# Kernel optimization log

Measured on AMD Instinct MI355X. Metric: run time of the kernel, lower is better.

## Reference

```python
import jax, jax.numpy as jnp
import numpy as np

B, L, C = 4, 8192, 256
HEADS = 1
DP = C // HEADS
FFN_HID = C * 2 * 4  # (d_model*2) * ffn_dim_expansion
EPS = 1e-5


def _layernorm(x, gamma, beta):
    mu = jnp.mean(x, axis=-1, keepdims=True)
    var = jnp.var(x, axis=-1, keepdims=True)
    return (x - mu) * jax.lax.rsqrt(var + EPS) * gamma + beta


def setup_inputs() -> dict:
    key = jax.random.key(0)
    ks = jax.random.split(key, 12)
    s = 0.02
    return {
        "source": jax.random.normal(ks[0], (B, L, C), jnp.float32),
        "target": jax.random.normal(ks[1], (B, L, C), jnp.float32),
        "Wq": jax.random.normal(ks[2], (C, C), jnp.float32) * s,
        "Wk": jax.random.normal(ks[3], (C, C), jnp.float32) * s,
        "Wv": jax.random.normal(ks[4], (C, C), jnp.float32) * s,
        "Wl": jax.random.normal(ks[5], (C, C), jnp.float32) * s,
        "gamma1": jnp.ones((C,), jnp.float32),
        "beta1": jnp.zeros((C,), jnp.float32),
        "W1": jax.random.normal(ks[6], (2 * C, FFN_HID), jnp.float32) * s,
        "b1": jnp.zeros((FFN_HID,), jnp.float32),
        "W2": jax.random.normal(ks[7], (FFN_HID, C), jnp.float32) * s,
        "b2": jnp.zeros((C,), jnp.float32),
        "gamma2": jnp.ones((C,), jnp.float32),
        "beta2": jnp.zeros((C,), jnp.float32),
        "h": 64,
        "w": 128,
    }


def reference(source, target, Wq, Wk, Wv, Wl, gamma1, beta1, W1, b1, W2, b2,
              gamma2, beta2, h, w):
    assert L == h * w
    q = (source @ Wq).reshape(B, L, HEADS, DP)
    k = (target @ Wk).reshape(B, L, HEADS, DP)
    v = (target @ Wv).reshape(B, L, HEADS, DP)
    k = jax.nn.softmax(k, axis=1)  # softmax over token dim
    context = jnp.einsum('bnhd,bnhe->bhde', q, k)   # small d×d per head
    attn = jnp.einsum('bhde,bnhe->bnhd', context, v).reshape(B, L, C)
    message = _layernorm(attn @ Wl, gamma1, beta1)
    hidden = jax.nn.gelu(jnp.concatenate([source, message], axis=-1) @ W1 + b1,
                         approximate=False)
    message = _layernorm(hidden @ W2 + b2, gamma2, beta2)
    return source + message
```

## Files before the change

### kernel.cpp

```cpp
#include <hip/hip_runtime.h>
#include <hip/hip_bf16.h>

typedef unsigned short u16;
typedef __attribute__((ext_vector_type(8))) short short8;
typedef __attribute__((ext_vector_type(4))) float f32x4;

#define B_    4
#define L_    8192
#define C_    256
#define BL_   (B_*L_)
#define BLC_  (BL_*C_)
#define FFN_  2048
#define EPS_  1e-5f

#define GLDS(dst, src) __builtin_amdgcn_global_load_lds( \
    (const __attribute__((address_space(1))) unsigned int*)(src), \
    (__attribute__((address_space(3))) unsigned int*)(dst), 16, 0, 0)

__device__ __forceinline__ float bf2f(u16 v) {
  union { unsigned int u; float f; } x; x.u = ((unsigned int)v) << 16; return x.f;
}
__device__ __forceinline__ u16 f2bf(float f) {
  union { float f; unsigned int u; } x; x.f = f;
  unsigned int lsb = (x.u >> 16) & 1u;
  return (u16)((x.u + 0x7fffu + lsb) >> 16);
}
__device__ __forceinline__ float gelu_f(float x) {
  float z = fabsf(x) * 0.70710678118654752f;
  float t = __builtin_amdgcn_rcpf(1.f + 0.3275911f * z);
  float p = ((((1.061405429f * t - 1.453152027f) * t + 1.421413741f) * t
              - 0.284496736f) * t + 0.254829592f) * t;
  float e = __expf(-z * z);
  float erfv = copysignf(1.f - p * e, x);
  return 0.5f * x * (1.f + erfv);
}

template<int MODE, int ACT, int SPLITK>
__launch_bounds__(256, 2)
__global__ void gemm_abt(const u16* __restrict__ A0, const u16* __restrict__ A1,
                         int SEL, int lda,
                         const u16* __restrict__ Bt,
                         const float* __restrict__ bias,
                         u16* __restrict__ Cb, float* __restrict__ Cf,
                         int M, int N, int K,
                         long sAb, long sBb, long sCb)
{
  __shared__ __align__(16) u16 As[2 * 128 * 32];
  __shared__ __align__(16) u16 Bs[2 * 128 * 32];

  const int mtiles = M >> 7;
  const int tile = blockIdx.x;
  const int mt0 = (tile % mtiles) << 7;
  const int nt0 = (tile / mtiles) << 7;
  const int kchunk = K / (int)gridDim.y;
  const int k0beg = blockIdx.y * kchunk;
  const int k0end = k0beg + kchunk;
  const int bz = blockIdx.z;
  A0 += (long)bz * sAb;  A1 += (long)bz * sAb;  Bt += (long)bz * sBb;

  const u16* Abase = (MODE == 2 && nt0 >= SEL) ? A1 : A0;

  const int tid  = threadIdx.x;
  const int wave = tid >> 6, lane = tid & 63;
  const int srow = lane >> 2;
  const int gq   = (lane & 3) ^ (srow & 3);
  const int frow = lane & 15;
  const int fq   = lane >> 4;
  const int fqx  = (fq ^ (frow & 3)) * 8;

  f32x4 zero = {0.f, 0.f, 0.f, 0.f};
  f32x4 acc[4][4];
#pragma unroll
  for (int i = 0; i < 4; i++)
#pragma unroll
    for (int j = 0; j < 4; j++) acc[i][j] = zero;

  const int wm = (wave & 1) * 64, wn = (wave >> 1) * 64;

  for (int k0 = k0beg; k0 < k0end; k0 += 64) {
    __syncthreads();
    const u16* Asrc;
    int ka;
    if (MODE == 1) {
      const bool lo = (k0 < SEL);
      Asrc = lo ? A0 : A1;
      ka = lo ? k0 : (k0 - SEL);
    } else { Asrc = Abase; ka = k0; }
#pragma unroll
    for (int h = 0; h < 2; h++) {
#pragma unroll
      for (int i = 0; i < 2; i++) {
        const int chunk = i * 4 + wave;
        GLDS(&As[h * 4096 + chunk * 512],
             Asrc + (long)(mt0 + chunk * 16 + srow) * lda + (ka + h * 32 + gq * 8));
        GLDS(&Bs[h * 4096 + chunk * 512],
             Bt + (long)(nt0 + chunk * 16 + srow) * K + (k0 + h * 32 + gq * 8));
      }
    }
    __syncthreads();
#pragma unroll
    for (int h = 0; h < 2; h++) {
      short8 af[4], bf[4];
#pragma unroll
      for (int t = 0; t < 4; t++)
        af[t] = *(const short8*)&As[h * 4096 + (wm + t * 16 + frow) * 32 + fqx];
#pragma unroll
      for (int t = 0; t < 4; t++)
        bf[t] = *(const short8*)&Bs[h * 4096 + (wn + t * 16 + frow) * 32 + fqx];
#pragma unroll
      for (int mt = 0; mt < 4; mt++)
#pragma unroll
        for (int nt = 0; nt < 4; nt++)
          acc[mt][nt] = __builtin_amdgcn_mfma_f32_16x16x32_bf16(af[mt], bf[nt], acc[mt][nt], 0, 0, 0);
    }
  }

  if (SPLITK) {
    float* Cp = Cf + (long)bz * sCb;
#pragma unroll
    for (int mt = 0; mt < 4; mt++)
#pragma unroll
      for (int r = 0; r < 4; r++) {
        const int row = mt0 + wm + mt * 16 + fq * 4 + r;
#pragma unroll
        for (int nt = 0; nt < 4; nt++)
          atomicAdd(&Cp[(long)row * N + nt0 + wn + nt * 16 + frow], acc[mt][nt][r]);
      }
  } else {
    u16* Cp = Cb + (long)bz * sCb;
    float bv[4];
#pragma unroll
    for (int nt = 0; nt < 4; nt++)
      bv[nt] = bias ? bias[nt0 + wn + nt * 16 + frow] : 0.f;
#pragma unroll
    for (int mt = 0; mt < 4; mt++)
#pragma unroll
      for (int r = 0; r < 4; r++) {
        const int row = mt0 + wm + mt * 16 + fq * 4 + r;
#pragma unroll
        for (int nt = 0; nt < 4; nt++) {
          float v = acc[mt][nt][r] + bv[nt];
          if (ACT == 1) v = gelu_f(v);
          Cp[(long)row * N + nt0 + wn + nt * 16 + frow] = f2bf(v);
        }
      }
  }
}

template<int CVTB, int OUTF>
__launch_bounds__(256, 3)
__global__ void gemm_ln(const u16* __restrict__ A, long sAb, int lda, int K,
                        const void* __restrict__ Btv, long sBb, int zshift,
                        const float* __restrict__ bias,
                        const float* __restrict__ gamma, const float* __restrict__ beta,
                        const float* __restrict__ src, void* __restrict__ outv,
                        long Moff)
{
  __shared__ __align__(16) u16 As[2 * 64 * 32];
  __shared__ __align__(16) u16 Bs[2 * 256 * 32];
  __shared__ float red_s[64][4], red_q[64][4];

  const int gm0 = blockIdx.x * 64;
  const int z = gm0 >> zshift;
  const int ml = gm0 - (z << zshift);
  A += (long)z * sAb + (long)ml * lda;
  const float* Bf = (const float*)Btv + (CVTB ? (long)z * sBb : 0);
  const u16*   Bb = (const u16*)Btv   + (CVTB ? 0 : (long)z * sBb);

  const int tid = threadIdx.x, wave = tid >> 6, lane = tid & 63;
  const int srow = lane >> 2, gq = (lane & 3) ^ (srow & 3);
  const int frow = lane & 15, fq = lane >> 4;
  const int fqx = (fq ^ (frow & 3)) * 8;
  const int wn = wave * 64;

  f32x4 zero = {0.f, 0.f, 0.f, 0.f};
  f32x4 acc[4][4];
#pragma unroll
  for (int i = 0; i < 4; i++)
#pragma unroll
    for (int j = 0; j < 4; j++) acc[i][j] = zero;

  for (int k0 = 0; k0 < K; k0 += 64) {
    __syncthreads();
#pragma unroll
    for (int h = 0; h < 2; h++) {
      GLDS(&As[h * 2048 + wave * 512],
           A + (long)(wave * 16 + srow) * lda + (k0 + h * 32 + gq * 8));
#pragma unroll
      for (int i = 0; i < 4; i++) {
        const int chunk = i * 4 + wave;
        if (CVTB) {
          const float* bp = Bf + (long)(chunk * 16 + srow) * K + (k0 + h * 32 + gq * 8);
          float4 p0 = *(const float4*)bp;
          float4 p1 = *(const float4*)(bp + 4);
          short8 w;
          w[0] = (short)f2bf(p0.x); w[1] = (short)f2bf(p0.y);
          w[2] = (short)f2bf(p0.z); w[3] = (short)f2bf(p0.w);
          w[4] = (short)f2bf(p1.x); w[5] = (short)f2bf(p1.y);
          w[6] = (short)f2bf(p1.z); w[7] = (short)f2bf(p1.w);
          *(short8*)&Bs[h * 8192 + chunk * 512 + srow * 32 + (lane & 3) * 8] = w;
        } else {
          GLDS(&Bs[h * 8192 + chunk * 512],
               Bb + (long)(chunk * 16 + srow) * K + (k0 + h * 32 + gq * 8));
        }
      }
    }
    __syncthreads();
#pragma unroll
    for (int h = 0; h < 2; h++) {
      short8 af[4], bf[4];
#pragma unroll
      for (int t = 0; t < 4; t++)
        af[t] = *(const short8*)&As[h * 2048 + (t * 16 + frow) * 32 + fqx];
#pragma unroll
      for (int t = 0; t < 4; t++)
        bf[t] = *(const short8*)&Bs[h * 8192 + (wn + t * 16 + frow) * 32 + fqx];
#pragma unroll
      for (int mt = 0; mt < 4; mt++)
#pragma unroll
        for (int nt = 0; nt < 4; nt++)
          acc[mt][nt] = __builtin_amdgcn_mfma_f32_16x16x32_bf16(af[mt], bf[nt], acc[mt][nt], 0, 0, 0);
    }
  }

  float gv[4], bv[4], b2v[4];
#pragma unroll
  for (int nt = 0; nt < 4; nt++) {
    const int col = wn + nt * 16 + frow;
    gv[nt] = gamma[col]; bv[nt] = beta[col];
    b2v[nt] = OUTF ? bias[col] : 0.f;
  }
#pragma unroll
  for (int mt = 0; mt < 4; mt++)
#pragma unroll
    for (int r = 0; r < 4; r++) {
      float s = 0.f, q = 0.f;
#pragma unroll
      for (int nt = 0; nt < 4; nt++) {
        float v = acc[mt][nt][r] + b2v[nt];
        acc[mt][nt][r] = v; s += v; q += v * v;
      }
#pragma unroll
      for (int m = 1; m < 16; m <<= 1) {
        s += __shfl_xor(s, m, 16); q += __shfl_xor(q, m, 16);
      }
      if (frow == 0) {
        const int row = mt * 16 + fq * 4 + r;
        red_s[row][wave] = s; red_q[row][wave] = q;
      }
    }
  __syncthreads();
#pragma unroll
  for (int mt = 0; mt < 4; mt++)
#pragma unroll
    for (int r = 0; r < 4; r++) {
      const int row = mt * 16 + fq * 4 + r;
      float4 ss = *(const float4*)red_s[row];
      float4 qq = *(const float4*)red_q[row];
      const float s = ss.x + ss.y + ss.z + ss.w;
      const float q = qq.x + qq.y + qq.z + qq.w;
      const float mu = s * (1.f / 256.f);
      const float var = q * (1.f / 256.f) - mu * mu;
      const float rs = 1.f / sqrtf(var + EPS_);
      const long grow = Moff + gm0 + row;
#pragma unroll
      for (int nt = 0; nt < 4; nt++) {
        const int col = wn + nt * 16 + frow;
        const float o = (acc[mt][nt][r] - mu) * rs * gv[nt] + bv[nt];
        if (OUTF)
          ((float*)outv)[grow * 256 + col] = o + src[grow * 256 + col];
        else
          ((u16*)outv)[grow * 256 + col] = f2bf(o);
      }
    }
}

__global__ void weightpack(const float* __restrict__ Wq, const float* __restrict__ Wk,
                           const float* __restrict__ Wv, const float* __restrict__ Wl,
                           const float* __restrict__ W1, const float* __restrict__ W2,
                           u16* __restrict__ WqC, u16* __restrict__ WlT,
                           u16* __restrict__ WqkvT, u16* __restrict__ W1T,
                           u16* __restrict__ W2T)
{
  __shared__ u16 t[32][33];
  const int bid = blockIdx.x, tx = threadIdx.x, ty = threadIdx.y;
  const float* in; u16* out; int Cc, R, bx, by;
  if (bid < 256) {
    const int w = bid >> 6, tt = bid & 63;
    bx = (tt & 7) * 32; by = (tt >> 3) * 32; Cc = 256; R = 256;
    if (w == 0) {
#pragma unroll
      for (int i = ty; i < 32; i += 8)
        WqC[(long)(by + i) * 256 + bx + tx] = f2bf(Wq[(long)(by + i) * 256 + bx + tx]);
      return;
    }
    in  = (w == 1) ? Wl : (w == 2) ? Wk : Wv;
    out = (w == 1) ? WlT : (w == 2) ? (WqkvT + 65536) : (WqkvT + 131072);
  } else if (bid < 1280) {
    const int l = bid - 256; bx = (l & 63) * 32; by = (l >> 6) * 32;
    in = W1; out = W1T; Cc = 2048; R = 512;
  } else {
    const int l = bid - 1280; bx = (l & 7) * 32; by = (l >> 3) * 32;
    in = W2; out = W2T; Cc = 256; R = 2048;
  }
#pragma unroll
  for (int i = ty; i < 32; i += 8)
    t[i][tx] = f2bf(in[(long)(by + i) * Cc + bx + tx]);
  __syncthreads();
#pragma unroll
  for (int i = ty; i < 32; i += 8)
    out[(long)(bx + i) * R + by + tx] = t[tx][i];
}

__global__ void castzero(const float* __restrict__ src, const float* __restrict__ tgt,
                         u16* __restrict__ srcB, u16* __restrict__ tgtB,
                         float* __restrict__ Mtf)
{
  const int x = blockIdx.x;
  if (x < BLC_ / 1024) {
    const float* in = blockIdx.y ? tgt : src;
    u16* out = blockIdx.y ? tgtB : srcB;
    const int i = (x * 256 + threadIdx.x) * 4;
    float4 v = *(const float4*)(in + i);
    ushort4 o; o.x = f2bf(v.x); o.y = f2bf(v.y); o.z = f2bf(v.z); o.w = f2bf(v.w);
    *(ushort4*)(out + i) = o;
  } else if (blockIdx.y == 0) {
    const int i = ((x - BLC_ / 1024) * 256 + threadIdx.x) * 4;
    float4 zv = {0.f, 0.f, 0.f, 0.f};
    *(float4*)(Mtf + i) = zv;
  }
}

__global__ void transQK(const u16* __restrict__ QKV,
                        u16* __restrict__ qlT, u16* __restrict__ kT)
{
  __shared__ u16 t[32][33];
  const int z = blockIdx.z, zb = z & 3;
  const u16* in = QKV + (long)zb * L_ * 768 + (z < 4 ? 0 : 256);
  u16* out = (z < 4 ? qlT : kT) + (long)zb * L_ * C_;
  const int bx = blockIdx.x * 32, by = blockIdx.y * 32;
  const int tx = threadIdx.x, ty = threadIdx.y;
#pragma unroll
  for (int i = ty; i < 32; i += 8)
    t[i][tx] = in[(long)(by + i) * 768 + bx + tx];
  __syncthreads();
#pragma unroll
  for (int i = ty; i < 32; i += 8)
    out[(long)(bx + i) * L_ + by + tx] = t[tx][i];
}

__global__ void softmax_rows(u16* __restrict__ data, int rowlen)
{
  const long base = (long)blockIdx.x * rowlen;
  const int tid = threadIdx.x, wave = tid >> 6, lane = tid & 63;
  __shared__ float red[4];

  float m = -3.4e38f;
  for (int i = tid; i < rowlen; i += 256) m = fmaxf(m, bf2f(data[base + i]));
#pragma unroll
  for (int off = 32; off; off >>= 1) m = fmaxf(m, __shfl_xor(m, off, 64));
  if (lane == 0) red[wave] = m;
  __syncthreads();
  m = fmaxf(fmaxf(red[0], red[1]), fmaxf(red[2], red[3]));
  __syncthreads();

  float s = 0.f;
  for (int i = tid; i < rowlen; i += 256) s += expf(bf2f(data[base + i]) - m);
#pragma unroll
  for (int off = 32; off; off >>= 1) s += __shfl_xor(s, off, 64);
  if (lane == 0) red[wave] = s;
  __syncthreads();
  const float inv = 1.f / (red[0] + red[1] + red[2] + red[3]);
  for (int i = tid; i < rowlen; i += 256)
    data[base + i] = f2bf(expf(bf2f(data[base + i]) - m) * inv);
}

extern "C" void kernel_launch(void* const* d_in, const int* in_sizes, int n_in,
                              void* d_out, int out_size, void* d_ws, size_t ws_size,
                              hipStream_t stream)
{
  const float* source = (const float*)d_in[0];
  const float* target = (const float*)d_in[1];
  const float* Wq     = (const float*)d_in[2];
  const float* Wk     = (const float*)d_in[3];
  const float* Wv     = (const float*)d_in[4];
  const float* Wl     = (const float*)d_in[5];
  const float* gamma1 = (const float*)d_in[6];
  const float* beta1  = (const float*)d_in[7];
  const float* W1     = (const float*)d_in[8];
  const float* b1     = (const float*)d_in[9];
  const float* W2     = (const float*)d_in[10];
  const float* b2     = (const float*)d_in[11];
  const float* gamma2 = (const float*)d_in[12];
  const float* beta2  = (const float*)d_in[13];
  (void)in_sizes; (void)n_in; (void)out_size;

  char* ws = (char*)d_ws;
  size_t off = 0;
  auto take = [&](size_t bytes) -> char* {
    char* p = ws + off; off += (bytes + 255) & ~(size_t)255; return p;
  };
  u16*   WqkvT = (u16*)take((size_t)768 * C_ * 2);
  u16*   WqC   = (u16*)take((size_t)C_ * C_ * 2);
  u16*   WlT   = (u16*)take((size_t)C_ * C_ * 2);
  u16*   W1T   = (u16*)take((size_t)FFN_ * 512 * 2);
  u16*   W2T   = (u16*)take((size_t)C_ * FFN_ * 2);
  float* Mtf   = (float*)take((size_t)B_ * C_ * C_ * 4);
  u16*   srcB  = (u16*)take((size_t)BLC_ * 2);
  u16*   msg   = (u16*)take((size_t)BLC_ * 2);
  const size_t ubase = off;
  u16*   tgtB  = (u16*)take((size_t)BLC_ * 2);
  u16*   QKV   = (u16*)take((size_t)BL_ * 768 * 2);
  u16*   qlT   = (u16*)take((size_t)BLC_ * 2);
  u16*   kT    = (u16*)take((size_t)BLC_ * 2);
  const size_t pool = off - ubase;
  u16*   hidden = (u16*)(ws + ubase);

  int nchunk = 1;
  for (; nchunk < 8; nchunk <<= 1) {
    size_t hid = ((size_t)BL_ / nchunk) * FFN_ * 2;
    size_t need = ubase + (hid > pool ? hid : pool);
    if (need <= ws_size) break;
  }
  const int Mc = BL_ / nchunk;

  dim3 tb(32, 8);
  weightpack<<<1792, tb, 0, stream>>>(Wq, Wk, Wv, Wl, W1, W2, WqC, WlT, WqkvT, W1T, W2T);
  castzero<<<dim3(BLC_ / 1024 + (B_ * C_ * C_) / 1024, 2), 256, 0, stream>>>(
      source, target, srcB, tgtB, Mtf);

  gemm_abt<0,0,0><<<4, 256, 0, stream>>>(
      WlT, WlT, 0, C_, WqC, nullptr, WqkvT, nullptr, C_, C_, C_, 0, 0, 0);

  gemm_abt<2,0,0><<<(BL_/128)*(768/128), 256, 0, stream>>>(
      srcB, tgtB, 256, C_, WqkvT, nullptr, QKV, nullptr, BL_, 768, C_, 0, 0, 0);

  transQK<<<dim3(8, L_/32, 8), tb, 0, stream>>>(QKV, qlT, kT);
  softmax_rows<<<B_*C_, 256, 0, stream>>>(kT, L_);

  gemm_abt<0,0,1><<<dim3(4, 16, B_), 256, 0, stream>>>(
      qlT, qlT, 0, L_, kT, nullptr, nullptr, Mtf, C_, C_, L_,
      (long)C_*L_, (long)C_*L_, (long)C_*C_);

  gemm_ln<1,0><<<BL_/64, 256, 0, stream>>>(
      QKV + 512, (long)L_*768, 768, 256, Mtf, (long)C_*C_, 13,
      nullptr, gamma1, beta1, nullptr, msg, 0);

  for (int ch = 0; ch < nchunk; ch++) {
    const long moff = (long)ch * Mc;
    gemm_abt<1,1,0><<<(Mc/128)*(FFN_/128), 256, 0, stream>>>(
        srcB + moff * C_, msg + moff * C_, 256, C_, W1T, b1, hidden, nullptr,
        Mc, FFN_, 512, 0, 0, 0);
    gemm_ln<0,1><<<Mc/64, 256, 0, stream>>>(
        hidden, 0, FFN_, FFN_, W2T, 0, 30,
        b2, gamma2, beta2, source, d_out, moff);
  }
}
```

Baseline: 419.3 us.

## Fuse key softmax into transpose, approximate GELU, and swizzle GEMM tile order

Removes the separate three-pass softmax kernel by computing exp of keys during the transpose, accumulating per-channel sums with atomics, and applying the reciprocal normalization as a scale in the split-K context GEMM epilogue. It also replaces the erf-polynomial GELU with a cheaper sigmoid-style approximation, and remaps GEMM tile indices into groups of eight for better L2 reuse. The softmax drops max subtraction, which risks overflow for large key values, and the GELU approximation changes numerics slightly. The sum buffer relies on the enlarged zeroing grid, which writes into Mtf's tail and spills into the padded sexp region placed right after it.

```diff
diff --git a/kernel.cpp b/kernel.cpp
--- a/kernel.cpp
+++ b/kernel.cpp
@@ -26,13 +26,11 @@
   return (u16)((x.u + 0x7fffu + lsb) >> 16);
 }
 __device__ __forceinline__ float gelu_f(float x) {
-  float z = fabsf(x) * 0.70710678118654752f;
-  float t = __builtin_amdgcn_rcpf(1.f + 0.3275911f * z);
-  float p = ((((1.061405429f * t - 1.453152027f) * t + 1.421413741f) * t
-              - 0.284496736f) * t + 0.254829592f) * t;
-  float e = __expf(-z * z);
-  float erfv = copysignf(1.f - p * e, x);
-  return 0.5f * x * (1.f + erfv);
+  float u = x * x;
+  float w = x * (2.3023879925f + 0.1029517046f * u);
+  float e = exp2f(w);
+  float r = __builtin_amdgcn_rcpf(1.f + e);
+  return x - x * r;
 }
 
 template<int MODE, int ACT, int SPLITK>
@@ -48,10 +46,17 @@
   __shared__ __align__(16) u16 As[2 * 128 * 32];
   __shared__ __align__(16) u16 Bs[2 * 128 * 32];
 
-  const int mtiles = M >> 7;
+  const int mtiles = M >> 7, ntiles = N >> 7;
   const int tile = blockIdx.x;
-  const int mt0 = (tile % mtiles) << 7;
-  const int nt0 = (tile / mtiles) << 7;
+  int mt0, nt0;
+  if ((mtiles & 7) == 0) {
+    const int x = tile & 7, g = tile >> 3;
+    mt0 = ((x * (mtiles >> 3)) + g / ntiles) << 7;
+    nt0 = (g % ntiles) << 7;
+  } else {
+    mt0 = (tile % mtiles) << 7;
+    nt0 = (tile / mtiles) << 7;
+  }
   const int kchunk = K / (int)gridDim.y;
   const int k0beg = blockIdx.y * kchunk;
   const int k0end = k0beg + kchunk;
@@ -117,6 +122,10 @@
 
   if (SPLITK) {
     float* Cp = Cf + (long)bz * sCb;
+    float sv[4];
+#pragma unroll
+    for (int nt = 0; nt < 4; nt++)
+      sv[nt] = bias ? (1.f / bias[(long)bz * N + nt0 + wn + nt * 16 + frow]) : 1.f;
 #pragma unroll
     for (int mt = 0; mt < 4; mt++)
 #pragma unroll
@@ -124,7 +133,8 @@
         const int row = mt0 + wm + mt * 16 + fq * 4 + r;
 #pragma unroll
         for (int nt = 0; nt < 4; nt++)
-          atomicAdd(&Cp[(long)row * N + nt0 + wn + nt * 16 + frow], acc[mt][nt][r]);
+          atomicAdd(&Cp[(long)row * N + nt0 + wn + nt * 16 + frow],
+                    acc[mt][nt][r] * sv[nt]);
       }
   } else {
     u16* Cp = Cb + (long)bz * sCb;
@@ -332,47 +342,35 @@
 }
 
 __global__ void transQK(const u16* __restrict__ QKV,
-                        u16* __restrict__ qlT, u16* __restrict__ kT)
+                        u16* __restrict__ qlT, u16* __restrict__ kT,
+                        float* __restrict__ sexp)
 {
   __shared__ u16 t[32][33];
   const int z = blockIdx.z, zb = z & 3;
-  const u16* in = QKV + (long)zb * L_ * 768 + (z < 4 ? 0 : 256);
-  u16* out = (z < 4 ? qlT : kT) + (long)zb * L_ * C_;
+  const bool isk = (z >= 4);
+  const u16* in = QKV + (long)zb * L_ * 768 + (isk ? 256 : 0);
+  u16* out = (isk ? kT : qlT) + (long)zb * L_ * C_;
   const int bx = blockIdx.x * 32, by = blockIdx.y * 32;
   const int tx = threadIdx.x, ty = threadIdx.y;
 #pragma unroll
   for (int i = ty; i < 32; i += 8)
     t[i][tx] = in[(long)(by + i) * 768 + bx + tx];
   __syncthreads();
-#pragma unroll
-  for (int i = ty; i < 32; i += 8)
-    out[(long)(bx + i) * L_ + by + tx] = t[tx][i];
-}
-
-__global__ void softmax_rows(u16* __restrict__ data, int rowlen)
-{
-  const long base = (long)blockIdx.x * rowlen;
-  const int tid = threadIdx.x, wave = tid >> 6, lane = tid & 63;
-  __shared__ float red[4];
-
-  float m = -3.4e38f;
-  for (int i = tid; i < rowlen; i += 256) m = fmaxf(m, bf2f(data[base + i]));
-#pragma unroll
-  for (int off = 32; off; off >>= 1) m = fmaxf(m, __shfl_xor(m, off, 64));
-  if (lane == 0) red[wave] = m;
-  __syncthreads();
-  m = fmaxf(fmaxf(red[0], red[1]), fmaxf(red[2], red[3]));
-  __syncthreads();
-
-  float s = 0.f;
-  for (int i = tid; i < rowlen; i += 256) s += expf(bf2f(data[base + i]) - m);
-#pragma unroll
-  for (int off = 32; off; off >>= 1) s += __shfl_xor(s, off, 64);
-  if (lane == 0) red[wave] = s;
-  __syncthreads();
-  const float inv = 1.f / (red[0] + red[1] + red[2] + red[3]);
-  for (int i = tid; i < rowlen; i += 256)
-    data[base + i] = f2bf(expf(bf2f(data[base + i]) - m) * inv);
+  if (isk) {
+#pragma unroll
+    for (int i = ty; i < 32; i += 8) {
+      float ex = __expf(bf2f(t[tx][i]));
+      out[(long)(bx + i) * L_ + by + tx] = f2bf(ex);
+      float ps = ex;
+#pragma unroll
+      for (int m = 1; m <= 16; m <<= 1) ps += __shfl_xor(ps, m, 32);
+      if (tx == 0) atomicAdd(&sexp[(long)zb * C_ + bx + i], ps);
+    }
+  } else {
+#pragma unroll
+    for (int i = ty; i < 32; i += 8)
+      out[(long)(bx + i) * L_ + by + tx] = t[tx][i];
+  }
 }
 
 extern "C" void kernel_launch(void* const* d_in, const int* in_sizes, int n_in,
@@ -406,6 +404,7 @@
   u16*   W1T   = (u16*)take((size_t)FFN_ * 512 * 2);
   u16*   W2T   = (u16*)take((size_t)C_ * FFN_ * 2);
   float* Mtf   = (float*)take((size_t)B_ * C_ * C_ * 4);
+  float* sexp  = (float*)take((size_t)B_ * C_ * 4);
   u16*   srcB  = (u16*)take((size_t)BLC_ * 2);
   u16*   msg   = (u16*)take((size_t)BLC_ * 2);
   const size_t ubase = off;
@@ -426,7 +425,7 @@
 
   dim3 tb(32, 8);
   weightpack<<<1792, tb, 0, stream>>>(Wq, Wk, Wv, Wl, W1, W2, WqC, WlT, WqkvT, W1T, W2T);
-  castzero<<<dim3(BLC_ / 1024 + (B_ * C_ * C_) / 1024, 2), 256, 0, stream>>>(
+  castzero<<<dim3(BLC_ / 1024 + (B_ * C_ * C_ + B_ * C_) / 1024, 2), 256, 0, stream>>>(
       source, target, srcB, tgtB, Mtf);
 
   gemm_abt<0,0,0><<<4, 256, 0, stream>>>(
@@ -435,11 +434,10 @@
   gemm_abt<2,0,0><<<(BL_/128)*(768/128), 256, 0, stream>>>(
       srcB, tgtB, 256, C_, WqkvT, nullptr, QKV, nullptr, BL_, 768, C_, 0, 0, 0);
 
-  transQK<<<dim3(8, L_/32, 8), tb, 0, stream>>>(QKV, qlT, kT);
-  softmax_rows<<<B_*C_, 256, 0, stream>>>(kT, L_);
+  transQK<<<dim3(8, L_/32, 8), tb, 0, stream>>>(QKV, qlT, kT, sexp);
 
   gemm_abt<0,0,1><<<dim3(4, 16, B_), 256, 0, stream>>>(
-      qlT, qlT, 0, L_, kT, nullptr, nullptr, Mtf, C_, C_, L_,
+      qlT, qlT, 0, L_, kT, sexp, nullptr, Mtf, C_, C_, L_,
       (long)C_*L_, (long)C_*L_, (long)C_*C_);
 
   gemm_ln<1,0><<<BL_/64, 256, 0, stream>>>(
```

New measurement: 534.2 us. +27.4%, slower.
